# Kernel tuning notes

Hardware: AMD Instinct MI355X
Metric: run time of the kernel (lower is better)

The kernel has to match this reference:

```python
import jax, jax.numpy as jnp
import numpy as np

D_MODEL = 1024
NHEAD = 16
HEAD_DIM = D_MODEL // NHEAD
D_FF = 4096
EPS = 1e-5


def _layer_norm(x, gamma, beta):
    mu = jnp.mean(x, axis=-1, keepdims=True)
    var = jnp.mean((x - mu) ** 2, axis=-1, keepdims=True)
    return (x - mu) * jax.lax.rsqrt(var + EPS) * gamma + beta


def setup_inputs() -> dict:
    key = jax.random.key(0)
    ks = jax.random.split(key, 12)
    B, S = 2, 2048
    s = lambda fan_in: 1.0 / np.sqrt(fan_in)
    return {
        "src": jax.random.normal(ks[0], (B, S, D_MODEL), dtype=jnp.float32),
        "attn_bias": jax.random.normal(ks[1], (NHEAD, S, S), dtype=jnp.float32) * 0.02,
        "qkv_w": jax.random.uniform(ks[2], (3 * D_MODEL, D_MODEL), minval=-s(D_MODEL), maxval=s(D_MODEL)),
        "qkv_b": jax.random.uniform(ks[3], (3 * D_MODEL,), minval=-s(D_MODEL), maxval=s(D_MODEL)),
        "out_w": jax.random.uniform(ks[4], (D_MODEL, D_MODEL), minval=-s(D_MODEL), maxval=s(D_MODEL)),
        "out_b": jax.random.uniform(ks[5], (D_MODEL,), minval=-s(D_MODEL), maxval=s(D_MODEL)),
        "lin1_w": jax.random.uniform(ks[6], (D_FF, D_MODEL), minval=-s(D_MODEL), maxval=s(D_MODEL)),
        "lin1_b": jax.random.uniform(ks[7], (D_FF,), minval=-s(D_MODEL), maxval=s(D_MODEL)),
        "lin2_w": jax.random.uniform(ks[8], (D_MODEL, D_FF), minval=-s(D_FF), maxval=s(D_FF)),
        "lin2_b": jax.random.uniform(ks[9], (D_MODEL,), minval=-s(D_FF), maxval=s(D_FF)),
        "ln1_g": jnp.ones((D_MODEL,)), "ln1_b": jnp.zeros((D_MODEL,)),
        "ln2_g": jnp.ones((D_MODEL,)), "ln2_b": jnp.zeros((D_MODEL,)),
    }


def reference(src, attn_bias, qkv_w, qkv_b, out_w, out_b, lin1_w, lin1_b,
              lin2_w, lin2_b, ln1_g, ln1_b, ln2_g, ln2_b):
    B, S, _ = src.shape
    qkv = src @ qkv_w.T + qkv_b                      # [B,S,3D]
    q, k, v = jnp.split(qkv, 3, axis=-1)
    q = q.reshape(B, S, NHEAD, HEAD_DIM)
    k = k.reshape(B, S, NHEAD, HEAD_DIM)
    v = v.reshape(B, S, NHEAD, HEAD_DIM)
    scores = jnp.einsum('bthd,bshd->bhts', q, k) / np.sqrt(HEAD_DIM)
    scores = scores + attn_bias[None]                # 3D bias -> broadcast over batch
    weights = jax.nn.softmax(scores, axis=-1)
    ctx = jnp.einsum('bhts,bshd->bthd', weights, v).reshape(B, S, D_MODEL)
    attn_out = ctx @ out_w.T + out_b
    x = _layer_norm(src + attn_out, ln1_g, ln1_b)
    ff = jax.nn.gelu(x @ lin1_w.T + lin1_b, approximate=False) @ lin2_w.T + lin2_b
    return _layer_norm(x + ff, ln2_g, ln2_b)
```

## Files before the change

kernel.cpp:

```cpp
#include <hip/hip_runtime.h>
#include <hip/hip_bf16.h>


#define DMODEL 1024
#define NHEAD  16
#define HD     64
#define DFF    4096
#define SEQ    2048
#define BATCH  2

using short8 = __attribute__((ext_vector_type(8))) short;
using f32x4  = __attribute__((ext_vector_type(4))) float;
typedef unsigned short bfu;

__device__ __forceinline__ bfu f2bf(float f) {
    unsigned int u = __float_as_uint(f);
    unsigned int r = (u + 0x7fffu + ((u >> 16) & 1u)) >> 16;
    return (bfu)r;
}

__device__ __forceinline__ float gelu_exact(float x) {
    return 0.5f * x * (1.0f + erff(x * 0.70710678118654752f));
}

__device__ __forceinline__ void gload16(const void* g, void* l) {
    __builtin_amdgcn_global_load_lds(
        (const __attribute__((address_space(1))) void*)g,
        (__attribute__((address_space(3))) void*)l, 16, 0, 0);
}

__device__ __forceinline__ int swz(int row, int colbyte) {
    return (row * 128 + colbyte) ^ ((row & 7) << 4);
}

__global__ __launch_bounds__(256) void cvt_f32_bf16(const float* __restrict__ in,
                                                    bfu* __restrict__ out, int n4) {
    int i = blockIdx.x * 256 + threadIdx.x;
    if (i >= n4) return;
    float4 v = *(const float4*)(in + (size_t)i * 4);
    uint2 o;
    o.x = (unsigned)f2bf(v.x) | ((unsigned)f2bf(v.y) << 16);
    o.y = (unsigned)f2bf(v.z) | ((unsigned)f2bf(v.w) << 16);
    *(uint2*)(out + (size_t)i * 4) = o;
}

template <int MODE>
__global__ __launch_bounds__(256) void gemm_bt(const bfu* __restrict__ A,
                                               const bfu* __restrict__ W,
                                               const float* __restrict__ bias,
                                               void* __restrict__ Cout,
                                               int M, int N, int K) {
    __shared__ __align__(16) bfu As[128 * 32];
    __shared__ __align__(16) bfu Bs[128 * 32];
    const int tid = threadIdx.x;
    const int wid = tid >> 6, lane = tid & 63;
    const int lg = lane >> 4, li = lane & 15;
    const int row0 = blockIdx.x * 128, col0 = blockIdx.y * 128;
    const int wr = (wid >> 1) * 64, wc = (wid & 1) * 64;
    f32x4 acc[4][4] = {};

    const int ch_row0 = (tid >> 2);
    const int ch_colb = (tid & 3) * 16;
    const bfu* Ag0 = A + (size_t)(row0 + ch_row0) * K + (ch_colb >> 1);
    const bfu* Ag1 = A + (size_t)(row0 + 64 + ch_row0) * K + (ch_colb >> 1);
    const bfu* Wg0 = W + (size_t)(col0 + ch_row0) * K + (ch_colb >> 1);
    const bfu* Wg1 = W + (size_t)(col0 + 64 + ch_row0) * K + (ch_colb >> 1);
    char* Al0 = (char*)As + wid * 1024;
    char* Al1 = (char*)As + 4096 + wid * 1024;
    char* Bl0 = (char*)Bs + wid * 1024;
    char* Bl1 = (char*)Bs + 4096 + wid * 1024;

    for (int k0 = 0; k0 < K; k0 += 32) {
        gload16(Ag0 + k0, Al0);
        gload16(Ag1 + k0, Al1);
        gload16(Wg0 + k0, Bl0);
        gload16(Wg1 + k0, Bl1);
        __syncthreads();
        short8 af[4], bf_[4];
        #pragma unroll
        for (int m = 0; m < 4; ++m)
            af[m] = *(const short8*)(As + (wr + m * 16 + li) * 32 + lg * 8);
        #pragma unroll
        for (int n = 0; n < 4; ++n)
            bf_[n] = *(const short8*)(Bs + (wc + n * 16 + li) * 32 + lg * 8);
        #pragma unroll
        for (int m = 0; m < 4; ++m)
            #pragma unroll
            for (int n = 0; n < 4; ++n)
                acc[m][n] = __builtin_amdgcn_mfma_f32_16x16x32_bf16(af[m], bf_[n], acc[m][n], 0, 0, 0);
        __syncthreads();
    }

    #pragma unroll
    for (int m = 0; m < 4; ++m) {
        #pragma unroll
        for (int n = 0; n < 4; ++n) {
            #pragma unroll
            for (int r = 0; r < 4; ++r) {
                int row = row0 + wr + m * 16 + lg * 4 + r;
                int col = col0 + wc + n * 16 + li;
                float v = acc[m][n][r] + bias[col];
                if (MODE == 2) v = gelu_exact(v);
                if (MODE == 1)
                    ((float*)Cout)[(size_t)row * N + col] = v;
                else
                    ((bfu*)Cout)[(size_t)row * N + col] = f2bf(v);
            }
        }
    }
}

__global__ __launch_bounds__(256) void attn_kernel(const bfu* __restrict__ qkv,
                                                   const float* __restrict__ bias,
                                                   bfu* __restrict__ ctx) {
    __shared__ __align__(16) bfu Qs[64 * 64];
    __shared__ __align__(16) bfu Ks[64 * 64];
    __shared__ __align__(16) bfu Vt[64 * 64];
    __shared__ __align__(16) bfu Ps[4 * 16 * 64];
    const int tid = threadIdx.x;
    const int wid = tid >> 6, lane = tid & 63;
    const int lg = lane >> 4, li = lane & 15;
    const int q0 = blockIdx.x * 64;
    const int bh = blockIdx.y;
    const int b = bh >> 4, h = bh & 15;
    const size_t tokbase = (size_t)b * SEQ;

    #pragma unroll
    for (int i = 0; i < 2; ++i) {
        int idx = (i * 256 + tid) * 8;
        int r = idx >> 6, c = idx & 63;
        uint4 v = *(const uint4*)(qkv + (tokbase + q0 + r) * 3072 + h * 64 + c);
        *(uint4*)((char*)Qs + swz(r, c * 2)) = v;
    }

    f32x4 o[4] = {};
    float mrow[4], lrow[4];
    #pragma unroll
    for (int r = 0; r < 4; ++r) { mrow[r] = -1e30f; lrow[r] = 0.f; }

    char* pbase = (char*)Ps + wid * 2048;
    const float* brow = bias + (size_t)h * SEQ * SEQ;
    const int qrbase = q0 + wid * 16 + lg * 4;

    for (int kt = 0; kt < SEQ; kt += 64) {
        #pragma unroll
        for (int i = 0; i < 2; ++i) {
            int idx = (i * 256 + tid) * 8;
            int r = idx >> 6, c = idx & 63;
            uint4 v = *(const uint4*)(qkv + (tokbase + kt + r) * 3072 + 1024 + h * 64 + c);
            *(uint4*)((char*)Ks + swz(r, c * 2)) = v;
        }
        #pragma unroll
        for (int i = 0; i < 2; ++i) {
            int d = lane;
            int jb = i * 4 + wid;
            bfu tmp[8];
            #pragma unroll
            for (int u = 0; u < 8; ++u)
                tmp[u] = qkv[(tokbase + kt + jb * 8 + u) * 3072 + 2048 + h * 64 + d];
            uint4 pv;
            pv.x = (unsigned)tmp[0] | ((unsigned)tmp[1] << 16);
            pv.y = (unsigned)tmp[2] | ((unsigned)tmp[3] << 16);
            pv.z = (unsigned)tmp[4] | ((unsigned)tmp[5] << 16);
            pv.w = (unsigned)tmp[6] | ((unsigned)tmp[7] << 16);
            *(uint4*)((char*)Vt + swz(d, jb * 16)) = pv;
        }
        float breg[4][4];
        #pragma unroll
        for (int r = 0; r < 4; ++r)
            #pragma unroll
            for (int nb = 0; nb < 4; ++nb)
                breg[r][nb] = brow[(size_t)(qrbase + r) * SEQ + kt + nb * 16 + li];
        __syncthreads();

        f32x4 s[4] = {};
        __builtin_amdgcn_s_setprio(1);
        #pragma unroll
        for (int cb = 0; cb < 2; ++cb) {
            short8 qa = *(const short8*)((char*)Qs + swz(wid * 16 + li, cb * 64 + lg * 16));
            short8 kf[4];
            #pragma unroll
            for (int nb = 0; nb < 4; ++nb)
                kf[nb] = *(const short8*)((char*)Ks + swz(nb * 16 + li, cb * 64 + lg * 16));
            #pragma unroll
            for (int nb = 0; nb < 4; ++nb)
                s[nb] = __builtin_amdgcn_mfma_f32_16x16x32_bf16(qa, kf[nb], s[nb], 0, 0, 0);
        }
        __builtin_amdgcn_s_setprio(0);

        #pragma unroll
        for (int r = 0; r < 4; ++r) {
            float sv[4];
            float mx = -1e30f;
            #pragma unroll
            for (int nb = 0; nb < 4; ++nb) {
                float v = s[nb][r] * 0.125f + breg[r][nb];
                sv[nb] = v;
                mx = fmaxf(mx, v);
            }
            #pragma unroll
            for (int off = 8; off; off >>= 1) mx = fmaxf(mx, __shfl_xor(mx, off));
            float mnew = fmaxf(mrow[r], mx);
            float sf = __expf(mrow[r] - mnew);
            mrow[r] = mnew;
            float rs = 0.f;
            #pragma unroll
            for (int nb = 0; nb < 4; ++nb) {
                float p = __expf(sv[nb] - mnew);
                rs += p;
                s[nb][r] = p;
            }
            #pragma unroll
            for (int off = 8; off; off >>= 1) rs += __shfl_xor(rs, off);
            lrow[r] = lrow[r] * sf + rs;
            #pragma unroll
            for (int dc = 0; dc < 4; ++dc) o[dc][r] *= sf;
        }

        #pragma unroll
        for (int nb = 0; nb < 4; ++nb)
            #pragma unroll
            for (int r = 0; r < 4; ++r)
                *(bfu*)(pbase + swz(lg * 4 + r, (nb * 16 + li) * 2)) = f2bf(s[nb][r]);

        __builtin_amdgcn_s_setprio(1);
        #pragma unroll
        for (int jb = 0; jb < 2; ++jb) {
            short8 pa = *(const short8*)(pbase + swz(li, jb * 64 + lg * 16));
            short8 vb[4];
            #pragma unroll
            for (int dc = 0; dc < 4; ++dc)
                vb[dc] = *(const short8*)((char*)Vt + swz(dc * 16 + li, jb * 64 + lg * 16));
            #pragma unroll
            for (int dc = 0; dc < 4; ++dc)
                o[dc] = __builtin_amdgcn_mfma_f32_16x16x32_bf16(pa, vb[dc], o[dc], 0, 0, 0);
        }
        __builtin_amdgcn_s_setprio(0);
        __syncthreads();
    }

    #pragma unroll
    for (int dc = 0; dc < 4; ++dc)
        #pragma unroll
        for (int r = 0; r < 4; ++r) {
            int qr = qrbase + r;
            int d = dc * 16 + li;
            float v = o[dc][r] / lrow[r];
            ctx[(tokbase + qr) * 1024 + h * 64 + d] = f2bf(v);
        }
}

__global__ __launch_bounds__(256) void residual_ln_kernel(const float* __restrict__ a,
                                                          const float* __restrict__ b,
                                                          const float* __restrict__ g,
                                                          const float* __restrict__ be,
                                                          float* __restrict__ xf,
                                                          bfu* __restrict__ xb) {
    const int row = blockIdx.x, t = threadIdx.x;
    const size_t off = (size_t)row * DMODEL + t * 4;
    float4 av = *(const float4*)(a + off);
    float4 bv = *(const float4*)(b + off);
    float4 v;
    v.x = av.x + bv.x; v.y = av.y + bv.y; v.z = av.z + bv.z; v.w = av.w + bv.w;
    float s  = v.x + v.y + v.z + v.w;
    float sq = v.x * v.x + v.y * v.y + v.z * v.z + v.w * v.w;
    #pragma unroll
    for (int o2 = 32; o2; o2 >>= 1) { s += __shfl_xor(s, o2); sq += __shfl_xor(sq, o2); }
    __shared__ float red[8];
    const int wid = t >> 6, lane = t & 63;
    if (lane == 0) { red[wid] = s; red[4 + wid] = sq; }
    __syncthreads();
    s  = red[0] + red[1] + red[2] + red[3];
    sq = red[4] + red[5] + red[6] + red[7];
    float mu  = s * (1.0f / DMODEL);
    float var = sq * (1.0f / DMODEL) - mu * mu;
    float rstd = rsqrtf(var + 1e-5f);
    float4 gv  = *(const float4*)(g + t * 4);
    float4 bev = *(const float4*)(be + t * 4);
    float4 ov;
    ov.x = (v.x - mu) * rstd * gv.x + bev.x;
    ov.y = (v.y - mu) * rstd * gv.y + bev.y;
    ov.z = (v.z - mu) * rstd * gv.z + bev.z;
    ov.w = (v.w - mu) * rstd * gv.w + bev.w;
    *(float4*)(xf + off) = ov;
    if (xb) {
        uint2 o;
        o.x = (unsigned)f2bf(ov.x) | ((unsigned)f2bf(ov.y) << 16);
        o.y = (unsigned)f2bf(ov.z) | ((unsigned)f2bf(ov.w) << 16);
        *(uint2*)(xb + off) = o;
    }
}

extern "C" void kernel_launch(void* const* d_in, const int* in_sizes, int n_in,
                              void* d_out, int out_size, void* d_ws, size_t ws_size,
                              hipStream_t stream) {
    const float* src    = (const float*)d_in[0];
    const float* abias  = (const float*)d_in[1];
    const float* qkv_w  = (const float*)d_in[2];
    const float* qkv_b  = (const float*)d_in[3];
    const float* out_w  = (const float*)d_in[4];
    const float* out_b  = (const float*)d_in[5];
    const float* lin1_w = (const float*)d_in[6];
    const float* lin1_b = (const float*)d_in[7];
    const float* lin2_w = (const float*)d_in[8];
    const float* lin2_b = (const float*)d_in[9];
    const float* ln1_g  = (const float*)d_in[10];
    const float* ln1_b  = (const float*)d_in[11];
    const float* ln2_g  = (const float*)d_in[12];
    const float* ln2_b  = (const float*)d_in[13];
    float* out = (float*)d_out;

    const int T = BATCH * SEQ;
    char* w = (char*)d_ws;
    auto take = [&](size_t bytes) { char* p = w; w += (bytes + 255) & ~(size_t)255; return p; };
    bfu*   src_bf  = (bfu*)take((size_t)T * DMODEL * 2);
    bfu*   qkvw_bf = (bfu*)take((size_t)3 * DMODEL * DMODEL * 2);
    bfu*   outw_bf = (bfu*)take((size_t)DMODEL * DMODEL * 2);
    bfu*   l1w_bf  = (bfu*)take((size_t)DFF * DMODEL * 2);
    bfu*   l2w_bf  = (bfu*)take((size_t)DMODEL * DFF * 2);
    bfu*   qkv_bf  = (bfu*)take((size_t)T * 3 * DMODEL * 2);
    bfu*   ctx_bf  = (bfu*)take((size_t)T * DMODEL * 2);
    float* attn_o  = (float*)take((size_t)T * DMODEL * 4);
    float* x_f     = (float*)take((size_t)T * DMODEL * 4);
    bfu*   x_bf    = (bfu*)take((size_t)T * DMODEL * 2);
    bfu*   h1_bf   = (bfu*)take((size_t)T * DFF * 2);
    float* ff_f    = (float*)take((size_t)T * DMODEL * 4);

    auto cvt = [&](const float* in, bfu* o_, size_t n) {
        int n4 = (int)(n / 4);
        cvt_f32_bf16<<<(n4 + 255) / 256, 256, 0, stream>>>(in, o_, n4);
    };
    cvt(src,    src_bf,  (size_t)T * DMODEL);
    cvt(qkv_w,  qkvw_bf, (size_t)3 * DMODEL * DMODEL);
    cvt(out_w,  outw_bf, (size_t)DMODEL * DMODEL);
    cvt(lin1_w, l1w_bf,  (size_t)DFF * DMODEL);
    cvt(lin2_w, l2w_bf,  (size_t)DMODEL * DFF);

    gemm_bt<0><<<dim3(T / 128, (3 * DMODEL) / 128), 256, 0, stream>>>(
        src_bf, qkvw_bf, qkv_b, qkv_bf, T, 3 * DMODEL, DMODEL);
    attn_kernel<<<dim3(SEQ / 64, BATCH * NHEAD), 256, 0, stream>>>(qkv_bf, abias, ctx_bf);
    gemm_bt<1><<<dim3(T / 128, DMODEL / 128), 256, 0, stream>>>(
        ctx_bf, outw_bf, out_b, attn_o, T, DMODEL, DMODEL);
    residual_ln_kernel<<<T, 256, 0, stream>>>(src, attn_o, ln1_g, ln1_b, x_f, x_bf);
    gemm_bt<2><<<dim3(T / 128, DFF / 128), 256, 0, stream>>>(
        x_bf, l1w_bf, lin1_b, h1_bf, T, DFF, DMODEL);
    gemm_bt<1><<<dim3(T / 128, DMODEL / 128), 256, 0, stream>>>(
        h1_bf, l2w_bf, lin2_b, ff_f, T, DMODEL, DFF);
    residual_ln_kernel<<<T, 256, 0, stream>>>(x_f, ff_f, ln2_g, ln2_b, out, nullptr);
}
```

Before: 417.1 us.

## Split-K narrow-tile GEMMs for N=1024 projections and prefetch K/V/bias in attention

The out-projection and FFN down-projection GEMMs now use 64-row tiles with split-K (2 and 4 ways). Each split writes fp32 partials, and the residual+LayerNorm kernel sums them and adds the bias. This is meant to raise the block count on these small-N GEMMs so the GPU's compute units are better filled. Separately, the attention kernel prefetches the next K, V and bias tiles into registers to overlap global loads with compute. The cost is extra partial-buffer traffic and higher register pressure in attention.

Measured after the change: 453.2 us. 1.09x slower.

```diff
diff --git a/kernel.cpp b/kernel.cpp
--- a/kernel.cpp
+++ b/kernel.cpp
@@ -8,6 +8,7 @@
 #define DFF    4096
 #define SEQ    2048
 #define BATCH  2
+#define TOKD   ((size_t)4096 * 1024)
 
 using short8 = __attribute__((ext_vector_type(8))) short;
 using f32x4  = __attribute__((ext_vector_type(4))) float;
@@ -44,67 +45,73 @@
     *(uint2*)(out + (size_t)i * 4) = o;
 }
 
-template <int MODE>
+template <int MODE, int BM, int SPLITK>
 __global__ __launch_bounds__(256) void gemm_bt(const bfu* __restrict__ A,
                                                const bfu* __restrict__ W,
                                                const float* __restrict__ bias,
                                                void* __restrict__ Cout,
                                                int M, int N, int K) {
-    __shared__ __align__(16) bfu As[128 * 32];
+    constexpr int MR = BM / 32;
+    __shared__ __align__(16) bfu As[BM * 32];
     __shared__ __align__(16) bfu Bs[128 * 32];
     const int tid = threadIdx.x;
     const int wid = tid >> 6, lane = tid & 63;
     const int lg = lane >> 4, li = lane & 15;
-    const int row0 = blockIdx.x * 128, col0 = blockIdx.y * 128;
-    const int wr = (wid >> 1) * 64, wc = (wid & 1) * 64;
-    f32x4 acc[4][4] = {};
-
-    const int ch_row0 = (tid >> 2);
-    const int ch_colb = (tid & 3) * 16;
-    const bfu* Ag0 = A + (size_t)(row0 + ch_row0) * K + (ch_colb >> 1);
-    const bfu* Ag1 = A + (size_t)(row0 + 64 + ch_row0) * K + (ch_colb >> 1);
-    const bfu* Wg0 = W + (size_t)(col0 + ch_row0) * K + (ch_colb >> 1);
-    const bfu* Wg1 = W + (size_t)(col0 + 64 + ch_row0) * K + (ch_colb >> 1);
+    const int row0 = blockIdx.x * BM, col0 = blockIdx.y * 128;
+    const int wr = (wid >> 1) * (BM / 2), wc = (wid & 1) * 64;
+    f32x4 acc[MR][4] = {};
+
+    const int kchunk = K / SPLITK;
+    const int kbeg = blockIdx.z * kchunk;
+
+    const int ch_row = tid >> 2;
+    const int ch_col = (tid & 3) * 8;
+    const bfu* Ag0 = A + (size_t)(row0 + ch_row) * K + kbeg + ch_col;
+    const bfu* Ag1 = A + (size_t)(row0 + 64 + ch_row) * K + kbeg + ch_col;
+    const bfu* Wg0 = W + (size_t)(col0 + ch_row) * K + kbeg + ch_col;
+    const bfu* Wg1 = W + (size_t)(col0 + 64 + ch_row) * K + kbeg + ch_col;
     char* Al0 = (char*)As + wid * 1024;
     char* Al1 = (char*)As + 4096 + wid * 1024;
     char* Bl0 = (char*)Bs + wid * 1024;
     char* Bl1 = (char*)Bs + 4096 + wid * 1024;
 
-    for (int k0 = 0; k0 < K; k0 += 32) {
+    for (int k0 = 0; k0 < kchunk; k0 += 32) {
         gload16(Ag0 + k0, Al0);
-        gload16(Ag1 + k0, Al1);
+        if constexpr (BM == 128) gload16(Ag1 + k0, Al1);
         gload16(Wg0 + k0, Bl0);
         gload16(Wg1 + k0, Bl1);
         __syncthreads();
-        short8 af[4], bf_[4];
-        #pragma unroll
-        for (int m = 0; m < 4; ++m)
+        short8 af[MR], bf_[4];
+        #pragma unroll
+        for (int m = 0; m < MR; ++m)
             af[m] = *(const short8*)(As + (wr + m * 16 + li) * 32 + lg * 8);
         #pragma unroll
         for (int n = 0; n < 4; ++n)
             bf_[n] = *(const short8*)(Bs + (wc + n * 16 + li) * 32 + lg * 8);
         #pragma unroll
-        for (int m = 0; m < 4; ++m)
+        for (int m = 0; m < MR; ++m)
             #pragma unroll
             for (int n = 0; n < 4; ++n)
                 acc[m][n] = __builtin_amdgcn_mfma_f32_16x16x32_bf16(af[m], bf_[n], acc[m][n], 0, 0, 0);
         __syncthreads();
     }
 
-    #pragma unroll
-    for (int m = 0; m < 4; ++m) {
+    float* Cp3 = (float*)Cout + (size_t)blockIdx.z * M * N;
+    #pragma unroll
+    for (int m = 0; m < MR; ++m) {
         #pragma unroll
         for (int n = 0; n < 4; ++n) {
             #pragma unroll
             for (int r = 0; r < 4; ++r) {
                 int row = row0 + wr + m * 16 + lg * 4 + r;
                 int col = col0 + wc + n * 16 + li;
-                float v = acc[m][n][r] + bias[col];
-                if (MODE == 2) v = gelu_exact(v);
-                if (MODE == 1)
-                    ((float*)Cout)[(size_t)row * N + col] = v;
-                else
+                if (MODE == 3) {
+                    Cp3[(size_t)row * N + col] = acc[m][n][r];
+                } else {
+                    float v = acc[m][n][r] + bias[col];
+                    if (MODE == 2) v = gelu_exact(v);
                     ((bfu*)Cout)[(size_t)row * N + col] = f2bf(v);
+                }
             }
         }
     }
@@ -125,12 +132,13 @@
     const int b = bh >> 4, h = bh & 15;
     const size_t tokbase = (size_t)b * SEQ;
 
+    const int srow = tid >> 3;
+    const int scol = (tid & 7) * 8;
+
     #pragma unroll
     for (int i = 0; i < 2; ++i) {
-        int idx = (i * 256 + tid) * 8;
-        int r = idx >> 6, c = idx & 63;
-        uint4 v = *(const uint4*)(qkv + (tokbase + q0 + r) * 3072 + h * 64 + c);
-        *(uint4*)((char*)Qs + swz(r, c * 2)) = v;
+        uint4 v = *(const uint4*)(qkv + (tokbase + q0 + i * 32 + srow) * 3072 + h * 64 + scol);
+        *(uint4*)((char*)Qs + swz(i * 32 + srow, scol * 2)) = v;
     }
 
     f32x4 o[4] = {};
@@ -142,35 +150,54 @@
     const float* brow = bias + (size_t)h * SEQ * SEQ;
     const int qrbase = q0 + wid * 16 + lg * 4;
 
+    uint4 kreg[2];
+    bfu vreg[16];
+    float bregN[4][4], breg[4][4];
+    #pragma unroll
+    for (int i = 0; i < 2; ++i)
+        kreg[i] = *(const uint4*)(qkv + (tokbase + 0 + i * 32 + srow) * 3072 + 1024 + h * 64 + scol);
+    #pragma unroll
+    for (int i = 0; i < 2; ++i)
+        #pragma unroll
+        for (int u = 0; u < 8; ++u)
+            vreg[i * 8 + u] = qkv[(tokbase + 0 + (i * 4 + wid) * 8 + u) * 3072 + 2048 + h * 64 + lane];
+    #pragma unroll
+    for (int r = 0; r < 4; ++r)
+        #pragma unroll
+        for (int nb = 0; nb < 4; ++nb)
+            bregN[r][nb] = brow[(size_t)(qrbase + r) * SEQ + 0 + nb * 16 + li];
+
     for (int kt = 0; kt < SEQ; kt += 64) {
+        const int ktn = (kt + 64 < SEQ) ? kt + 64 : kt;
+
+        #pragma unroll
+        for (int r = 0; r < 4; ++r)
+            #pragma unroll
+            for (int nb = 0; nb < 4; ++nb)
+                breg[r][nb] = bregN[r][nb];
+
+        #pragma unroll
+        for (int i = 0; i < 2; ++i)
+            *(uint4*)((char*)Ks + swz(i * 32 + srow, scol * 2)) = kreg[i];
         #pragma unroll
         for (int i = 0; i < 2; ++i) {
-            int idx = (i * 256 + tid) * 8;
-            int r = idx >> 6, c = idx & 63;
-            uint4 v = *(const uint4*)(qkv + (tokbase + kt + r) * 3072 + 1024 + h * 64 + c);
-            *(uint4*)((char*)Ks + swz(r, c * 2)) = v;
-        }
-        #pragma unroll
-        for (int i = 0; i < 2; ++i) {
-            int d = lane;
-            int jb = i * 4 + wid;
-            bfu tmp[8];
+            uint4 pv;
+            pv.x = (unsigned)vreg[i * 8 + 0] | ((unsigned)vreg[i * 8 + 1] << 16);
+            pv.y = (unsigned)vreg[i * 8 + 2] | ((unsigned)vreg[i * 8 + 3] << 16);
+            pv.z = (unsigned)vreg[i * 8 + 4] | ((unsigned)vreg[i * 8 + 5] << 16);
+            pv.w = (unsigned)vreg[i * 8 + 6] | ((unsigned)vreg[i * 8 + 7] << 16);
+            *(uint4*)((char*)Vt + swz(lane, (i * 4 + wid) * 16)) = pv;
+        }
+
+        #pragma unroll
+        for (int i = 0; i < 2; ++i)
+            kreg[i] = *(const uint4*)(qkv + (tokbase + ktn + i * 32 + srow) * 3072 + 1024 + h * 64 + scol);
+        #pragma unroll
+        for (int i = 0; i < 2; ++i)
             #pragma unroll
             for (int u = 0; u < 8; ++u)
-                tmp[u] = qkv[(tokbase + kt + jb * 8 + u) * 3072 + 2048 + h * 64 + d];
-            uint4 pv;
-            pv.x = (unsigned)tmp[0] | ((unsigned)tmp[1] << 16);
-            pv.y = (unsigned)tmp[2] | ((unsigned)tmp[3] << 16);
-            pv.z = (unsigned)tmp[4] | ((unsigned)tmp[5] << 16);
-            pv.w = (unsigned)tmp[6] | ((unsigned)tmp[7] << 16);
-            *(uint4*)((char*)Vt + swz(d, jb * 16)) = pv;
-        }
-        float breg[4][4];
-        #pragma unroll
-        for (int r = 0; r < 4; ++r)
-            #pragma unroll
-            for (int nb = 0; nb < 4; ++nb)
-                breg[r][nb] = brow[(size_t)(qrbase + r) * SEQ + kt + nb * 16 + li];
+                vreg[i * 8 + u] = qkv[(tokbase + ktn + (i * 4 + wid) * 8 + u) * 3072 + 2048 + h * 64 + lane];
+
         __syncthreads();
 
         f32x4 s[4] = {};
@@ -218,6 +245,12 @@
         }
 
         #pragma unroll
+        for (int r = 0; r < 4; ++r)
+            #pragma unroll
+            for (int nb = 0; nb < 4; ++nb)
+                bregN[r][nb] = brow[(size_t)(qrbase + r) * SEQ + ktn + nb * 16 + li];
+
+        #pragma unroll
         for (int nb = 0; nb < 4; ++nb)
             #pragma unroll
             for (int r = 0; r < 4; ++r)
@@ -250,18 +283,25 @@
         }
 }
 
-__global__ __launch_bounds__(256) void residual_ln_kernel(const float* __restrict__ a,
-                                                          const float* __restrict__ b,
-                                                          const float* __restrict__ g,
-                                                          const float* __restrict__ be,
-                                                          float* __restrict__ xf,
-                                                          bfu* __restrict__ xb) {
+template <int P>
+__global__ __launch_bounds__(256) void residual_lnP(const float* __restrict__ a,
+                                                    const float* __restrict__ parts,
+                                                    const float* __restrict__ pbias,
+                                                    const float* __restrict__ g,
+                                                    const float* __restrict__ be,
+                                                    float* __restrict__ xf,
+                                                    bfu* __restrict__ xb) {
     const int row = blockIdx.x, t = threadIdx.x;
     const size_t off = (size_t)row * DMODEL + t * 4;
-    float4 av = *(const float4*)(a + off);
-    float4 bv = *(const float4*)(b + off);
-    float4 v;
-    v.x = av.x + bv.x; v.y = av.y + bv.y; v.z = av.z + bv.z; v.w = av.w + bv.w;
+    float4 v = *(const float4*)(a + off);
+    #pragma unroll
+    for (int i = 0; i < P; ++i) {
+        float4 p = *(const float4*)(parts + i * TOKD + off);
+        v.x += p.x; v.y += p.y; v.z += p.z; v.w += p.w;
+    }
+    float4 pb = *(const float4*)(pbias + t * 4);
+    v.x += pb.x; v.y += pb.y; v.z += pb.z; v.w += pb.w;
+
     float s  = v.x + v.y + v.z + v.w;
     float sq = v.x * v.x + v.y * v.y + v.z * v.z + v.w * v.w;
     #pragma unroll
@@ -320,11 +360,11 @@
     bfu*   l2w_bf  = (bfu*)take((size_t)DMODEL * DFF * 2);
     bfu*   qkv_bf  = (bfu*)take((size_t)T * 3 * DMODEL * 2);
     bfu*   ctx_bf  = (bfu*)take((size_t)T * DMODEL * 2);
-    float* attn_o  = (float*)take((size_t)T * DMODEL * 4);
+    float* outp_p  = (float*)take((size_t)2 * T * DMODEL * 4);
     float* x_f     = (float*)take((size_t)T * DMODEL * 4);
     bfu*   x_bf    = (bfu*)take((size_t)T * DMODEL * 2);
     bfu*   h1_bf   = (bfu*)take((size_t)T * DFF * 2);
-    float* ff_f    = (float*)take((size_t)T * DMODEL * 4);
+    float* l2_p    = (float*)take((size_t)4 * T * DMODEL * 4);
 
     auto cvt = [&](const float* in, bfu* o_, size_t n) {
         int n4 = (int)(n / 4);
@@ -336,15 +376,15 @@
     cvt(lin1_w, l1w_bf,  (size_t)DFF * DMODEL);
     cvt(lin2_w, l2w_bf,  (size_t)DMODEL * DFF);
 
-    gemm_bt<0><<<dim3(T / 128, (3 * DMODEL) / 128), 256, 0, stream>>>(
+    gemm_bt<0, 128, 1><<<dim3(T / 128, (3 * DMODEL) / 128, 1), 256, 0, stream>>>(
         src_bf, qkvw_bf, qkv_b, qkv_bf, T, 3 * DMODEL, DMODEL);
     attn_kernel<<<dim3(SEQ / 64, BATCH * NHEAD), 256, 0, stream>>>(qkv_bf, abias, ctx_bf);
-    gemm_bt<1><<<dim3(T / 128, DMODEL / 128), 256, 0, stream>>>(
-        ctx_bf, outw_bf, out_b, attn_o, T, DMODEL, DMODEL);
-    residual_ln_kernel<<<T, 256, 0, stream>>>(src, attn_o, ln1_g, ln1_b, x_f, x_bf);
-    gemm_bt<2><<<dim3(T / 128, DFF / 128), 256, 0, stream>>>(
+    gemm_bt<3, 64, 2><<<dim3(T / 64, DMODEL / 128, 2), 256, 0, stream>>>(
+        ctx_bf, outw_bf, nullptr, outp_p, T, DMODEL, DMODEL);
+    residual_lnP<2><<<T, 256, 0, stream>>>(src, outp_p, out_b, ln1_g, ln1_b, x_f, x_bf);
+    gemm_bt<2, 128, 1><<<dim3(T / 128, DFF / 128, 1), 256, 0, stream>>>(
         x_bf, l1w_bf, lin1_b, h1_bf, T, DFF, DMODEL);
-    gemm_bt<1><<<dim3(T / 128, DMODEL / 128), 256, 0, stream>>>(
-        h1_bf, l2w_bf, lin2_b, ff_f, T, DMODEL, DFF);
-    residual_ln_kernel<<<T, 256, 0, stream>>>(x_f, ff_f, ln2_g, ln2_b, out, nullptr);
-}
+    gemm_bt<3, 64, 4><<<dim3(T / 64, DMODEL / 128, 4), 256, 0, stream>>>(
+        h1_bf, l2w_bf, nullptr, l2_p, T, DMODEL, DFF);
+    residual_lnP<4><<<T, 256, 0, stream>>>(x_f, l2_p, lin2_b, ln2_g, ln2_b, out, nullptr);
+}
```
